# Kernel tuning notes

Measured on AMD Instinct MI355X. Metric: run time of the kernel, lower is better.

Reference implementation:

```python
import jax, jax.numpy as jnp
import numpy as np

B, TQ, TK, D, V = 16, 64, 512, 256, 32000


def setup_inputs() -> dict:
    key = jax.random.key(0)
    k = jax.random.split(key, 8)
    return {
        "domainslots": jax.random.normal(k[0], (B, TQ, D), jnp.float32),
        "out_states": jax.random.normal(k[1], (B, TQ, D), jnp.float32),
        "context": jax.random.normal(k[2], (B, TK, D), jnp.float32),
        "context_plain": jax.random.randint(k[3], (B, TK), 0, V, jnp.int64 if jax.config.jax_enable_x64 else jnp.int32),
        "W_state": jax.random.normal(k[4], (D, V), jnp.float32) * 0.02,
        "b_state": jnp.zeros((V,), jnp.float32),
        "W_gen": jax.random.normal(k[5], (3 * D, 1), jnp.float32) * 0.02,
        "b_gen": jnp.zeros((1,), jnp.float32),
    }


def reference(domainslots, out_states, context, context_plain, W_state, b_state, W_gen, b_gen):
    d = out_states.shape[-1]
    # pointer attention: softmax(Q K^T / sqrt(d)) over context  -> [B, TQ, TK]
    scores = jnp.einsum("bqd,bkd->bqk", out_states, context) / jnp.sqrt(jnp.asarray(d, out_states.dtype))
    pointer_attn = jax.nn.softmax(scores, axis=-1)

    # generation distribution over vocab  -> [B, TQ, V]
    p_state_vocab = jax.nn.softmax(out_states @ W_state + b_state, axis=-1)

    # copy distribution: scatter-add attention mass onto source token ids
    b_idx = jnp.arange(B)[:, None, None]           # [B,1,1]
    q_idx = jnp.arange(TQ)[None, :, None]          # [1,TQ,1]
    v_idx = context_plain[:, None, :]              # [B,1,TK] broadcast over TQ
    p_state_ptr = jnp.zeros((B, TQ, V), p_state_vocab.dtype).at[b_idx, q_idx, v_idx].add(pointer_attn)

    # attention-weighted context vector  -> [B, TQ, D]
    context_vec = jnp.einsum("bqk,bkd->bqd", pointer_attn, context)

    # generation gate  -> [B, TQ, 1]
    p_gen_vec = jnp.concatenate([out_states, context_vec, domainslots], axis=-1)
    p_state_gen = jax.nn.sigmoid(p_gen_vec @ W_gen + b_gen)

    p_state_out = p_state_gen * p_state_vocab + (1.0 - p_state_gen) * p_state_ptr
    return jnp.log(p_state_out)
```

## Files before the change

kernel.cpp:

```cpp
#include <hip/hip_runtime.h>
#include <math.h>

typedef short short8 __attribute__((ext_vector_type(8)));
typedef float f32x4 __attribute__((ext_vector_type(4)));

#define B_ 16
#define TQ_ 64
#define TK_ 512
#define D_ 256
#define V_ 32000
#define M_ (B_ * TQ_)

__device__ __forceinline__ unsigned short f2bf(float x) {
    unsigned int u = __float_as_uint(x);
    unsigned int r = (u + 0x7fffu + ((u >> 16) & 1u)) >> 16;
    return (unsigned short)r;
}

__device__ __forceinline__ void gload_lds16(const void* g, void* l) {
    __builtin_amdgcn_global_load_lds(
        (const __attribute__((address_space(1))) void*)g,
        (__attribute__((address_space(3))) void*)l, 16, 0, 0);
}

__global__ __launch_bounds__(256) void dedup_kernel(
    const int* __restrict__ cp, int* __restrict__ nexta, int* __restrict__ leader)
{
    __shared__ __align__(16) int c[TK_];
    const int b = blockIdx.x, tid = threadIdx.x;
    c[tid] = cp[b * TK_ + tid];
    c[tid + 256] = cp[b * TK_ + 256 + tid];
    __syncthreads();
    for (int k = tid; k < TK_; k += 256) {
        const int v = c[k];
        int fm = 1024, nx = 1024;
#pragma unroll 8
        for (int j0 = 0; j0 < TK_; j0 += 4) {
            const int4 q = *(const int4*)&c[j0];
            if (q.x == v) { fm = min(fm, j0);     if (j0     > k) nx = min(nx, j0);     }
            if (q.y == v) { fm = min(fm, j0 + 1); if (j0 + 1 > k) nx = min(nx, j0 + 1); }
            if (q.z == v) { fm = min(fm, j0 + 2); if (j0 + 2 > k) nx = min(nx, j0 + 2); }
            if (q.w == v) { fm = min(fm, j0 + 3); if (j0 + 3 > k) nx = min(nx, j0 + 3); }
        }
        nexta[b * TK_ + k] = (nx < 1024) ? nx : -1;
        leader[b * TK_ + k] = (fm == k) ? 1 : 0;
    }
}

__global__ __launch_bounds__(256) void conv_a_kernel(
    const float* __restrict__ A, unsigned short* __restrict__ Ab)
{
    const int i = (blockIdx.x * 256 + threadIdx.x) * 4;
    const float4 v = *(const float4*)&A[i];
    ushort4 o;
    o.x = f2bf(v.x); o.y = f2bf(v.y); o.z = f2bf(v.z); o.w = f2bf(v.w);
    *(ushort4*)&Ab[i] = o;
}

__global__ __launch_bounds__(256) void conv_w_kernel(
    const float* __restrict__ W, unsigned short* __restrict__ Wt)
{
    __shared__ float tile[64][65];
    const int tid = threadIdx.x;
    const int k0 = (blockIdx.x & 3) * 64;
    const int n0 = (blockIdx.x >> 2) * 64;
#pragma unroll
    for (int i = 0; i < 16; i++) {
        const int r = i * 4 + (tid >> 6), cc = tid & 63;
        tile[r][cc] = W[(k0 + r) * V_ + n0 + cc];
    }
    __syncthreads();
#pragma unroll
    for (int i = 0; i < 4; i++) {
        const int nl = i * 16 + (tid >> 4);
        const int kq = (tid & 15) * 4;
        ushort4 o;
        o.x = f2bf(tile[kq + 0][nl]);
        o.y = f2bf(tile[kq + 1][nl]);
        o.z = f2bf(tile[kq + 2][nl]);
        o.w = f2bf(tile[kq + 3][nl]);
        *(ushort4*)&Wt[(n0 + nl) * D_ + k0 + kq] = o;
    }
}

__global__ __launch_bounds__(256) void conv_c_kernel(
    const float* __restrict__ ctx, unsigned short* __restrict__ Cb,
    unsigned short* __restrict__ Ct)
{
    __shared__ float tile[64][65];
    const int tid = threadIdx.x;
    const int b = blockIdx.x >> 5;
    const int r5 = blockIdx.x & 31;
    const int k0 = (r5 >> 2) * 64;
    const int d0 = (r5 & 3) * 64;
#pragma unroll
    for (int i = 0; i < 16; i++) {
        const int r = i * 4 + (tid >> 6), cc = tid & 63;
        const float v = ctx[((b * TK_) + k0 + r) * D_ + d0 + cc];
        tile[r][cc] = v;
        Cb[((b * TK_) + k0 + r) * D_ + d0 + cc] = f2bf(v);
    }
    __syncthreads();
#pragma unroll
    for (int i = 0; i < 4; i++) {
        const int dl = i * 16 + (tid >> 4);
        const int kq = (tid & 15) * 4;
        ushort4 o;
        o.x = f2bf(tile[kq + 0][dl]);
        o.y = f2bf(tile[kq + 1][dl]);
        o.z = f2bf(tile[kq + 2][dl]);
        o.w = f2bf(tile[kq + 3][dl]);
        *(ushort4*)&Ct[((b * D_) + d0 + dl) * TK_ + k0 + kq] = o;
    }
}

template <int LDA, int LDB, int KTOT>
__global__ __launch_bounds__(256) void gemm_small(
    const unsigned short* __restrict__ A,
    const unsigned short* __restrict__ Bt,
    float* __restrict__ C, int ldc, int nchunks, int btrows, float scale)
{
    __shared__ short Al[64][72];
    __shared__ short Bl[128][72];
    const int tid = threadIdx.x;
    const int b = blockIdx.x / nchunks;
    const int n0 = (blockIdx.x % nchunks) * 128;
    A += (size_t)b * 64 * LDA;
    Bt += (size_t)b * btrows * LDB;
    C += (size_t)b * 64 * ldc;

    const int wid = tid >> 6;
    const int lane = tid & 63;
    const int wm = wid & 1, wn = wid >> 1;
    const int quad = lane >> 4, l15 = lane & 15;

    f32x4 acc[2][4];
#pragma unroll
    for (int i = 0; i < 2; i++)
#pragma unroll
        for (int j = 0; j < 4; j++) acc[i][j] = f32x4{0.f, 0.f, 0.f, 0.f};

    for (int k0 = 0; k0 < KTOT; k0 += 64) {
        __syncthreads();
#pragma unroll
        for (int i = 0; i < 2; i++) {
            const int c = tid + i * 256;
            const int r = c >> 3, kc = (c & 7) * 8;
            *(uint4*)&Al[r][kc] = *(const uint4*)&A[r * LDA + k0 + kc];
        }
#pragma unroll
        for (int i = 0; i < 4; i++) {
            const int c = tid + i * 256;
            const int r = c >> 3, kc = (c & 7) * 8;
            *(uint4*)&Bl[r][kc] = *(const uint4*)&Bt[(n0 + r) * LDB + k0 + kc];
        }
        __syncthreads();
#pragma unroll
        for (int ks = 0; ks < 64; ks += 32) {
            short8 af[2], bf[4];
#pragma unroll
            for (int mt = 0; mt < 2; mt++)
                af[mt] = *(const short8*)&Al[wm * 32 + mt * 16 + l15][ks + quad * 8];
#pragma unroll
            for (int nt = 0; nt < 4; nt++)
                bf[nt] = *(const short8*)&Bl[wn * 64 + nt * 16 + l15][ks + quad * 8];
#pragma unroll
            for (int mt = 0; mt < 2; mt++)
#pragma unroll
                for (int nt = 0; nt < 4; nt++)
                    acc[mt][nt] = __builtin_amdgcn_mfma_f32_16x16x32_bf16(
                        af[mt], bf[nt], acc[mt][nt], 0, 0, 0);
        }
    }
#pragma unroll
    for (int mt = 0; mt < 2; mt++)
#pragma unroll
        for (int nt = 0; nt < 4; nt++)
#pragma unroll
            for (int r = 0; r < 4; r++) {
                const int rl = wm * 32 + mt * 16 + quad * 4 + r;
                const int col = n0 + wn * 64 + nt * 16 + l15;
                C[rl * ldc + col] = acc[mt][nt][r] * scale;
            }
}

__global__ __launch_bounds__(256) void softmax_kernel(
    float* __restrict__ S, unsigned short* __restrict__ Pb)
{
    const int w = threadIdx.x >> 6, lane = threadIdx.x & 63;
    const int row = blockIdx.x * 4 + w;
    float v[8], m = -1e30f;
#pragma unroll
    for (int j = 0; j < 8; j++) { v[j] = S[row * TK_ + lane + 64 * j]; m = fmaxf(m, v[j]); }
#pragma unroll
    for (int off = 32; off; off >>= 1) m = fmaxf(m, __shfl_xor(m, off));
    float s = 0.f;
#pragma unroll
    for (int j = 0; j < 8; j++) { v[j] = __expf(v[j] - m); s += v[j]; }
#pragma unroll
    for (int off = 32; off; off >>= 1) s += __shfl_xor(s, off);
    const float inv = 1.0f / s;
#pragma unroll
    for (int j = 0; j < 8; j++) {
        const float p = v[j] * inv;
        S[row * TK_ + lane + 64 * j] = p;
        Pb[row * TK_ + lane + 64 * j] = f2bf(p);
    }
}

__global__ __launch_bounds__(256) void pgen_kernel(
    const float* __restrict__ os, const float* __restrict__ cv,
    const float* __restrict__ dm, const float* __restrict__ W_gen,
    const float* __restrict__ b_gen, float* __restrict__ pg)
{
    const int w = threadIdx.x >> 6, lane = threadIdx.x & 63;
    const int row = blockIdx.x * 4 + w;
    const int d4 = lane * 4;
    const float4 o4 = *(const float4*)&os[row * D_ + d4];
    const float4 c4 = *(const float4*)&cv[row * D_ + d4];
    const float4 m4 = *(const float4*)&dm[row * D_ + d4];
    const float4 w0 = *(const float4*)&W_gen[d4];
    const float4 w1 = *(const float4*)&W_gen[D_ + d4];
    const float4 w2 = *(const float4*)&W_gen[2 * D_ + d4];
    float p = o4.x * w0.x + o4.y * w0.y + o4.z * w0.z + o4.w * w0.w
            + c4.x * w1.x + c4.y * w1.y + c4.z * w1.z + c4.w * w1.w
            + m4.x * w2.x + m4.y * w2.y + m4.z * w2.z + m4.w * w2.w;
#pragma unroll
    for (int off = 32; off; off >>= 1) p += __shfl_xor(p, off);
    if (lane == 0) pg[row] = 1.0f / (1.0f + __expf(-(p + b_gen[0])));
}

template <int PASS>
__global__ __launch_bounds__(256) void gemm_vocab(
    const unsigned short* __restrict__ A,
    const unsigned short* __restrict__ Bt,
    const float* __restrict__ b_state,
    const float* __restrict__ rc,
    float* __restrict__ Z,
    float* __restrict__ out)
{
    __shared__ short Al[128][256];
    __shared__ short Bl[128][256];

    const int tid = threadIdx.x;
    const int swz = (blockIdx.x & 7) * 250 + (blockIdx.x >> 3);
    const int m0 = (swz & 7) * 128;
    const int n0 = (swz >> 3) * 128;

    const int wid = tid >> 6, lane = tid & 63;
    const int wm = wid & 1, wn = wid >> 1;
    const int quad = lane >> 4, l15 = lane & 15;

    const int rpar = lane >> 5;
    const int slot = lane & 31;
#pragma unroll
    for (int j = 0; j < 16; j++) {
        const int c = j * 4 + wid;
        const int r = c * 2 + rpar;
        const int ksrc = ((slot ^ (r & 7)) << 3);
        gload_lds16(&A[(size_t)(m0 + r) * D_ + ksrc], &Al[c * 2][0]);
        gload_lds16(&Bt[(size_t)(n0 + r) * D_ + ksrc], &Bl[c * 2][0]);
    }
    __syncthreads();

    f32x4 acc[4][4];
#pragma unroll
    for (int i = 0; i < 4; i++)
#pragma unroll
        for (int j = 0; j < 4; j++) acc[i][j] = f32x4{0.f, 0.f, 0.f, 0.f};

#pragma unroll
    for (int ks = 0; ks < D_; ks += 32) {
        short8 af[4], bf[4];
#pragma unroll
        for (int mt = 0; mt < 4; mt++) {
            const int row = wm * 64 + mt * 16 + l15;
            af[mt] = *(const short8*)&Al[row][(ks + quad * 8) ^ ((l15 & 7) << 3)];
        }
#pragma unroll
        for (int nt = 0; nt < 4; nt++) {
            const int row = wn * 64 + nt * 16 + l15;
            bf[nt] = *(const short8*)&Bl[row][(ks + quad * 8) ^ ((l15 & 7) << 3)];
        }
#pragma unroll
        for (int mt = 0; mt < 4; mt++)
#pragma unroll
            for (int nt = 0; nt < 4; nt++)
                acc[mt][nt] = __builtin_amdgcn_mfma_f32_16x16x32_bf16(
                    af[mt], bf[nt], acc[mt][nt], 0, 0, 0);
    }

    float bcol[4];
#pragma unroll
    for (int nt = 0; nt < 4; nt++)
        bcol[nt] = b_state[n0 + wn * 64 + nt * 16 + l15];

    if (PASS == 0) {
#pragma unroll
        for (int mt = 0; mt < 4; mt++) {
            float rs[4] = {0.f, 0.f, 0.f, 0.f};
#pragma unroll
            for (int nt = 0; nt < 4; nt++)
#pragma unroll
                for (int r = 0; r < 4; r++)
                    rs[r] += __expf(acc[mt][nt][r] + bcol[nt]);
#pragma unroll
            for (int r = 0; r < 4; r++) {
                float v = rs[r];
                v += __shfl_xor(v, 1);
                v += __shfl_xor(v, 2);
                v += __shfl_xor(v, 4);
                v += __shfl_xor(v, 8);
                if (l15 == 0)
                    atomicAdd(&Z[m0 + wm * 64 + mt * 16 + quad * 4 + r], v);
            }
        }
    } else {
        float rcv[4][4];
#pragma unroll
        for (int mt = 0; mt < 4; mt++)
#pragma unroll
            for (int r = 0; r < 4; r++)
                rcv[mt][r] = rc[m0 + wm * 64 + mt * 16 + quad * 4 + r];
#pragma unroll
        for (int mt = 0; mt < 4; mt++)
#pragma unroll
            for (int nt = 0; nt < 4; nt++)
#pragma unroll
                for (int r = 0; r < 4; r++) {
                    const int row = wm * 64 + mt * 16 + quad * 4 + r;
                    const int col = wn * 64 + nt * 16 + l15;
                    out[(size_t)(m0 + row) * V_ + n0 + col] =
                        acc[mt][nt][r] + bcol[nt] + rcv[mt][r];
                }
    }
}

__global__ __launch_bounds__(256) void rowconst_kernel(
    const float* __restrict__ pg, const float* __restrict__ Z, float* __restrict__ rcv)
{
    const int r = blockIdx.x * 256 + threadIdx.x;
    rcv[r] = logf(pg[r]) - logf(Z[r]);
}

__global__ __launch_bounds__(256) void fixup_kernel(
    const int* __restrict__ cp, const int* __restrict__ nexta,
    const int* __restrict__ leader, const float* __restrict__ attn,
    const float* __restrict__ pg, float* __restrict__ out)
{
    const int t = blockIdx.x * 256 + threadIdx.x;
    const int row = t >> 9, k = t & 511;
    const int b = row >> 6;
    if (!leader[b * TK_ + k]) return;
    float a = attn[row * TK_ + k];
    int j = nexta[b * TK_ + k];
    while (j >= 0) { a += attn[row * TK_ + j]; j = nexta[b * TK_ + j]; }
    const float val = (1.0f - pg[row]) * a;
    const int v = cp[b * TK_ + k];
    const size_t idx = (size_t)row * V_ + v;
    out[idx] = logf(expf(out[idx]) + val);
}

extern "C" void kernel_launch(void* const* d_in, const int* in_sizes, int n_in,
                              void* d_out, int out_size, void* d_ws, size_t ws_size,
                              hipStream_t stream)
{
    const float* domainslots = (const float*)d_in[0];
    const float* out_states  = (const float*)d_in[1];
    const float* context     = (const float*)d_in[2];
    const int*   cp          = (const int*)d_in[3];
    const float* W_state     = (const float*)d_in[4];
    const float* b_state     = (const float*)d_in[5];
    const float* W_gen       = (const float*)d_in[6];
    const float* b_gen       = (const float*)d_in[7];
    float* out = (float*)d_out;
    char* ws = (char*)d_ws;

    float* Z      = (float*)(ws);
    float* pg     = (float*)(ws + 4096);
    float* rc     = (float*)(ws + 8192);
    float* S      = (float*)(ws + 12288);
    int* nexta    = (int*)(ws + 2109440);
    int* leader   = (int*)(ws + 2142208);
    unsigned short* Ab = (unsigned short*)(ws + 2174976);
    unsigned short* Wt = (unsigned short*)(ws + 2699264);
    unsigned short* Cb = (unsigned short*)(ws + 19083264);
    unsigned short* Ct = (unsigned short*)(ws + 23277568);
    unsigned short* Pb = (unsigned short*)(ws + 27471872);
    float* cv     = (float*)(ws + 28520448);

    hipMemsetAsync(Z, 0, M_ * sizeof(float), stream);
    dedup_kernel<<<B_, 256, 0, stream>>>(cp, nexta, leader);
    conv_a_kernel<<<(M_ * D_) / 1024, 256, 0, stream>>>(out_states, Ab);
    conv_w_kernel<<<(D_ / 64) * (V_ / 64), 256, 0, stream>>>(W_state, Wt);
    conv_c_kernel<<<B_ * 32, 256, 0, stream>>>(context, Cb, Ct);

    gemm_small<D_, D_, D_><<<B_ * 4, 256, 0, stream>>>(Ab, Cb, S, TK_, 4, TK_, 0.0625f);
    softmax_kernel<<<M_ / 4, 256, 0, stream>>>(S, Pb);
    gemm_small<TK_, TK_, TK_><<<B_ * 2, 256, 0, stream>>>(Pb, Ct, cv, D_, 2, D_, 1.0f);
    pgen_kernel<<<M_ / 4, 256, 0, stream>>>(out_states, cv, domainslots, W_gen, b_gen, pg);

    gemm_vocab<0><<<(M_ / 128) * (V_ / 128), 256, 0, stream>>>(Ab, Wt, b_state, nullptr, Z, nullptr);
    rowconst_kernel<<<M_ / 256, 256, 0, stream>>>(pg, Z, rc);
    gemm_vocab<1><<<(M_ / 128) * (V_ / 128), 256, 0, stream>>>(Ab, Wt, b_state, rc, nullptr, out);
    fixup_kernel<<<(M_ * TK_) / 256, 256, 0, stream>>>(cp, nexta, leader, S, pg, out);
}
```

Measured before the change: 342.2 us.

## Double-buffer K-chunks in vocab GEMM and fold row constant into epilogue

The vocab GEMM no longer loads the full 128x256 A and B tiles into LDS before computing. It now streams 64-wide K chunks through a double buffer, prefetching the next chunk while MFMAs run on the current one. This cuts LDS use from 128KB to 64KB per block, which may allow more blocks per CU and overlaps load latency with compute. The separate rowconst kernel is removed: each pass-1 thread now computes log(pg) - log(Z) itself. That saves a launch but repeats the logs across all column blocks.

```diff
diff --git a/kernel.cpp b/kernel.cpp
--- a/kernel.cpp
+++ b/kernel.cpp
@@ -235,12 +235,12 @@
     const unsigned short* __restrict__ A,
     const unsigned short* __restrict__ Bt,
     const float* __restrict__ b_state,
-    const float* __restrict__ rc,
+    const float* __restrict__ pg,
     float* __restrict__ Z,
     float* __restrict__ out)
 {
-    __shared__ short Al[128][256];
-    __shared__ short Bl[128][256];
+    __shared__ short Al[2][128][64];
+    __shared__ short Bl[2][128][64];
 
     const int tid = threadIdx.x;
     const int swz = (blockIdx.x & 7) * 250 + (blockIdx.x >> 3);
@@ -250,44 +250,64 @@
     const int wid = tid >> 6, lane = tid & 63;
     const int wm = wid & 1, wn = wid >> 1;
     const int quad = lane >> 4, l15 = lane & 15;
-
-    const int rpar = lane >> 5;
-    const int slot = lane & 31;
-#pragma unroll
-    for (int j = 0; j < 16; j++) {
+    const int srow = lane >> 3;
+    const int scolz = ((lane & 7) ^ srow) << 3;
+
+    const unsigned short* Ag = A + (size_t)m0 * D_;
+    const unsigned short* Bg = Bt + (size_t)n0 * D_;
+
+    f32x4 acc[4][4];
+#pragma unroll
+    for (int i = 0; i < 4; i++)
+#pragma unroll
+        for (int j = 0; j < 4; j++) acc[i][j] = f32x4{0.f, 0.f, 0.f, 0.f};
+
+#pragma unroll
+    for (int j = 0; j < 4; j++) {
         const int c = j * 4 + wid;
-        const int r = c * 2 + rpar;
-        const int ksrc = ((slot ^ (r & 7)) << 3);
-        gload_lds16(&A[(size_t)(m0 + r) * D_ + ksrc], &Al[c * 2][0]);
-        gload_lds16(&Bt[(size_t)(n0 + r) * D_ + ksrc], &Bl[c * 2][0]);
-    }
-    __syncthreads();
-
-    f32x4 acc[4][4];
-#pragma unroll
-    for (int i = 0; i < 4; i++)
-#pragma unroll
-        for (int j = 0; j < 4; j++) acc[i][j] = f32x4{0.f, 0.f, 0.f, 0.f};
-
-#pragma unroll
-    for (int ks = 0; ks < D_; ks += 32) {
-        short8 af[4], bf[4];
-#pragma unroll
-        for (int mt = 0; mt < 4; mt++) {
-            const int row = wm * 64 + mt * 16 + l15;
-            af[mt] = *(const short8*)&Al[row][(ks + quad * 8) ^ ((l15 & 7) << 3)];
-        }
-#pragma unroll
-        for (int nt = 0; nt < 4; nt++) {
-            const int row = wn * 64 + nt * 16 + l15;
-            bf[nt] = *(const short8*)&Bl[row][(ks + quad * 8) ^ ((l15 & 7) << 3)];
-        }
-#pragma unroll
-        for (int mt = 0; mt < 4; mt++)
-#pragma unroll
-            for (int nt = 0; nt < 4; nt++)
-                acc[mt][nt] = __builtin_amdgcn_mfma_f32_16x16x32_bf16(
-                    af[mt], bf[nt], acc[mt][nt], 0, 0, 0);
+        const int r = c * 8 + srow;
+        gload_lds16(&Ag[(size_t)r * D_ + scolz], &Al[0][c * 8][0]);
+        gload_lds16(&Bg[(size_t)r * D_ + scolz], &Bl[0][c * 8][0]);
+    }
+
+#pragma unroll
+    for (int t = 0; t < 4; t++) {
+        const int cur = t & 1;
+        if (t < 3) {
+            const int k0n = (t + 1) * 64;
+#pragma unroll
+            for (int j = 0; j < 4; j++) {
+                const int c = j * 4 + wid;
+                const int r = c * 8 + srow;
+                gload_lds16(&Ag[(size_t)r * D_ + k0n + scolz], &Al[cur ^ 1][c * 8][0]);
+                gload_lds16(&Bg[(size_t)r * D_ + k0n + scolz], &Bl[cur ^ 1][c * 8][0]);
+            }
+            asm volatile("s_waitcnt vmcnt(8)" ::: "memory");
+        } else {
+            asm volatile("s_waitcnt vmcnt(0)" ::: "memory");
+        }
+        __builtin_amdgcn_s_barrier();
+#pragma unroll
+        for (int ks = 0; ks < 64; ks += 32) {
+            short8 af[4], bf[4];
+#pragma unroll
+            for (int mt = 0; mt < 4; mt++) {
+                const int row = wm * 64 + mt * 16 + l15;
+                af[mt] = *(const short8*)&Al[cur][row][(ks + quad * 8) ^ ((l15 & 7) << 3)];
+            }
+#pragma unroll
+            for (int nt = 0; nt < 4; nt++) {
+                const int row = wn * 64 + nt * 16 + l15;
+                bf[nt] = *(const short8*)&Bl[cur][row][(ks + quad * 8) ^ ((l15 & 7) << 3)];
+            }
+#pragma unroll
+            for (int mt = 0; mt < 4; mt++)
+#pragma unroll
+                for (int nt = 0; nt < 4; nt++)
+                    acc[mt][nt] = __builtin_amdgcn_mfma_f32_16x16x32_bf16(
+                        af[mt], bf[nt], acc[mt][nt], 0, 0, 0);
+        }
+        __builtin_amdgcn_s_barrier();
     }
 
     float bcol[4];
@@ -320,8 +340,10 @@
 #pragma unroll
         for (int mt = 0; mt < 4; mt++)
 #pragma unroll
-            for (int r = 0; r < 4; r++)
-                rcv[mt][r] = rc[m0 + wm * 64 + mt * 16 + quad * 4 + r];
+            for (int r = 0; r < 4; r++) {
+                const int row = m0 + wm * 64 + mt * 16 + quad * 4 + r;
+                rcv[mt][r] = logf(pg[row]) - logf(Z[row]);
+            }
 #pragma unroll
         for (int mt = 0; mt < 4; mt++)
 #pragma unroll
@@ -334,13 +356,6 @@
                         acc[mt][nt][r] + bcol[nt] + rcv[mt][r];
                 }
     }
-}
-
-__global__ __launch_bounds__(256) void rowconst_kernel(
-    const float* __restrict__ pg, const float* __restrict__ Z, float* __restrict__ rcv)
-{
-    const int r = blockIdx.x * 256 + threadIdx.x;
-    rcv[r] = logf(pg[r]) - logf(Z[r]);
 }
 
 __global__ __launch_bounds__(256) void fixup_kernel(
@@ -378,7 +393,6 @@
 
     float* Z      = (float*)(ws);
     float* pg     = (float*)(ws + 4096);
-    float* rc     = (float*)(ws + 8192);
     float* S      = (float*)(ws + 12288);
     int* nexta    = (int*)(ws + 2109440);
     int* leader   = (int*)(ws + 2142208);
@@ -401,7 +415,6 @@
     pgen_kernel<<<M_ / 4, 256, 0, stream>>>(out_states, cv, domainslots, W_gen, b_gen, pg);
 
     gemm_vocab<0><<<(M_ / 128) * (V_ / 128), 256, 0, stream>>>(Ab, Wt, b_state, nullptr, Z, nullptr);
-    rowconst_kernel<<<M_ / 256, 256, 0, stream>>>(pg, Z, rc);
-    gemm_vocab<1><<<(M_ / 128) * (V_ / 128), 256, 0, stream>>>(Ab, Wt, b_state, rc, nullptr, out);
+    gemm_vocab<1><<<(M_ / 128) * (V_ / 128), 256, 0, stream>>>(Ab, Wt, b_state, pg, Z, out);
     fixup_kernel<<<(M_ * TK_) / 256, 256, 0, stream>>>(cp, nexta, leader, S, pg, out);
 }
```

New measurement: 327.4 us. -4.3%, faster.
